# Optimization experiments

Hardware: AMD Instinct MI355X
Metric: run time of the kernel (lower is better)

## Reference

```python
import jax, jax.numpy as jnp
import numpy as np

B, A, T, NH, NEMB = 8, 32, 64, 256, 256
E = A * (A - 1)  # fully-connected directed edges, no self-loops


def _onehot_edges():
    # NRI-style: rows of off-diagonal pairs (send i -> recv j, i != j)
    send_idx, recv_idx = [], []
    for i in range(A):
        for j in range(A):
            if i != j:
                send_idx.append(i)
                recv_idx.append(j)
    rel_send = jax.nn.one_hot(jnp.array(send_idx), A, dtype=jnp.float32)
    rel_rec = jax.nn.one_hot(jnp.array(recv_idx), A, dtype=jnp.float32)
    return rel_rec, rel_send


def setup_inputs() -> dict:
    key = jax.random.key(0)
    k1, k2, k3 = jax.random.split(key, 3)
    h = jax.random.normal(k1, (B, A, T, NH), dtype=jnp.float32)
    rel_rec, rel_send = _onehot_edges()
    # nn.Linear(2*n_h, n_emb): W [n_emb, 2*n_h], b [n_emb]
    lim = 1.0 / np.sqrt(2 * NH)
    W = jax.random.uniform(k2, (NEMB, 2 * NH), minval=-lim, maxval=lim, dtype=jnp.float32)
    b = jax.random.uniform(k3, (NEMB,), minval=-lim, maxval=lim, dtype=jnp.float32)
    return {"h": h, "rel_rec": rel_rec, "rel_send": rel_send, "W": W, "b": b}


def reference(h, rel_rec, rel_send, W, b):
    # h: [B, A, T, NH]; rel_rec/rel_send: [E, A] one-hot selectors
    # Equivalent to reshape->batched matmul->reshape in the torch code,
    # expressed as a single contraction over atoms.
    receivers = jnp.einsum('ea,bath->beth', rel_rec, h)   # [B, E, T, NH]
    senders = jnp.einsum('ea,bath->beth', rel_send, h)    # [B, E, T, NH]
    edges = jnp.concatenate([senders, receivers], axis=-1)  # [B, E, T, 2*NH]
    return jnp.einsum('betf,of->beto', edges, W) + b        # [B, E, T, NEMB]
```

## Files before the change

kernel.cpp:

```cpp
#include <hip/hip_runtime.h>
#include <hip/hip_bf16.h>

using f32x4  = __attribute__((ext_vector_type(4))) float;
using bf16x8 = __attribute__((ext_vector_type(8))) short;
using s16x4  = __attribute__((ext_vector_type(4))) short;

constexpr int kB  = 8;
constexpr int kA  = 32;
constexpr int kT  = 64;
constexpr int kNH = 256;
constexpr int kNE = 256;
constexpr int kE  = kA * (kA - 1);
constexpr int kM  = kB * kA * kT;
constexpr int kK  = kNH;
constexpr int kN  = 2 * kNE;

__device__ __forceinline__ unsigned short rne_bf16(float f) {
    unsigned int u = __float_as_uint(f);
    u += 0x7fffu + ((u >> 16) & 1u);
    return (unsigned short)(u >> 16);
}
__device__ __forceinline__ float bf16_f32(unsigned short h) {
    return __uint_as_float(((unsigned int)h) << 16);
}
__device__ __forceinline__ void split3(float x, unsigned short& h, unsigned short& m,
                                       unsigned short& l) {
    h = rne_bf16(x);
    float r1 = x - bf16_f32(h);
    m = rne_bf16(r1);
    float r2 = r1 - bf16_f32(m);
    l = rne_bf16(r2);
}

__global__ __launch_bounds__(256) void k_split_h(const float* __restrict__ src,
                                                 unsigned short* __restrict__ d1,
                                                 unsigned short* __restrict__ d2,
                                                 unsigned short* __restrict__ d3) {
    int idx = blockIdx.x * 256 + threadIdx.x;
    f32x4 v = ((const f32x4*)src)[idx];
    s16x4 o1, o2, o3;
#pragma unroll
    for (int j = 0; j < 4; ++j) {
        unsigned short h, m, l;
        split3(v[j], h, m, l);
        o1[j] = (short)h; o2[j] = (short)m; o3[j] = (short)l;
    }
    *(s16x4*)(d1 + (size_t)idx * 4) = o1;
    *(s16x4*)(d2 + (size_t)idx * 4) = o2;
    *(s16x4*)(d3 + (size_t)idx * 4) = o3;
}

__global__ __launch_bounds__(256) void k_split_w(const float* __restrict__ W,
                                                 unsigned short* __restrict__ d1,
                                                 unsigned short* __restrict__ d2,
                                                 unsigned short* __restrict__ d3,
                                                 const float* __restrict__ rel_rec,
                                                 const float* __restrict__ rel_send,
                                                 int* __restrict__ ij2e) {
    int idx = blockIdx.x * 256 + threadIdx.x;
    int n  = idx >> 6;
    int k4 = (idx & 63) << 2;
    const float* s = (n < kNE) ? (W + (size_t)n * (2 * kNH) + k4)
                               : (W + (size_t)(n - kNE) * (2 * kNH) + kNH + k4);
    f32x4 v = *(const f32x4*)s;
    s16x4 o1, o2, o3;
#pragma unroll
    for (int j = 0; j < 4; ++j) {
        unsigned short h, m, l;
        split3(v[j], h, m, l);
        o1[j] = (short)h; o2[j] = (short)m; o3[j] = (short)l;
    }
    size_t off = (size_t)n * kK + k4;
    *(s16x4*)(d1 + off) = o1;
    *(s16x4*)(d2 + off) = o2;
    *(s16x4*)(d3 + off) = o3;

    if (blockIdx.x < 4) {
        int e = blockIdx.x * 256 + threadIdx.x;
        if (e < kE) {
            int ir = 0, is = 0;
            for (int a = 0; a < kA; ++a) {
                if (rel_rec[(size_t)e * kA + a]  > 0.5f) ir = a;
                if (rel_send[(size_t)e * kA + a] > 0.5f) is = a;
            }
            ij2e[is * kA + ir] = e;
        }
    }
}

#define GLL(g, l) __builtin_amdgcn_global_load_lds( \
    (const __attribute__((address_space(1))) void*)(g), \
    (__attribute__((address_space(3))) void*)(l), 16, 0, 0)

__global__ __launch_bounds__(256) void k_gemm3(const unsigned short* __restrict__ Ah,
                                               const unsigned short* __restrict__ Am,
                                               const unsigned short* __restrict__ Al,
                                               const unsigned short* __restrict__ Bh,
                                               const unsigned short* __restrict__ Bm,
                                               const unsigned short* __restrict__ Bl,
                                               float* __restrict__ P) {
    __shared__ unsigned short sAh[128 * 32], sAm[128 * 32], sAl[128 * 32];
    __shared__ unsigned short sBh[128 * 32], sBm[128 * 32], sBl[128 * 32];
    const int tid  = threadIdx.x;
    const int lane = tid & 63;
    const int wave = tid >> 6;
    const int wr = wave >> 1, wc = wave & 1;
    const int bid = blockIdx.x;
    const int bm  = (bid & 7) * 16 + ((bid >> 3) & 15);
    const int bn  = bid >> 7;

    const int sr   = tid >> 2;
    const int scb  = (tid & 3) << 4;
    const int scbs = scb ^ (((sr >> 1) & 3) << 4);
    const size_t rA  = (size_t)(bm * 128 + sr) * kK + (scbs >> 1);
    const size_t rB  = (size_t)(bn * 128 + sr) * kK + (scbs >> 1);
    const size_t rA1 = rA + (size_t)64 * kK;
    const size_t rB1 = rB + (size_t)64 * kK;
    const int l0 = tid * 8, l1 = 64 * 32 + tid * 8;

    const int fr  = lane & 15;
    const int fkb = (lane >> 4) << 4;
    const int swz = ((fr >> 1) & 3) << 4;

    f32x4 acc[4][4] = {};

    for (int kt = 0; kt < kK / 32; ++kt) {
        const int kk = kt * 32;
        __syncthreads();
        GLL(Ah + rA + kk, sAh + l0);  GLL(Ah + rA1 + kk, sAh + l1);
        GLL(Am + rA + kk, sAm + l0);  GLL(Am + rA1 + kk, sAm + l1);
        GLL(Al + rA + kk, sAl + l0);  GLL(Al + rA1 + kk, sAl + l1);
        GLL(Bh + rB + kk, sBh + l0);  GLL(Bh + rB1 + kk, sBh + l1);
        GLL(Bm + rB + kk, sBm + l0);  GLL(Bm + rB1 + kk, sBm + l1);
        GLL(Bl + rB + kk, sBl + l0);  GLL(Bl + rB1 + kk, sBl + l1);
        __syncthreads();

        bf16x8 ah[4], am[4], al[4], bh[4], bmf[4], bl[4];
#pragma unroll
        for (int mi = 0; mi < 4; ++mi) {
            int row = wr * 64 + mi * 16 + fr;
            int off = row * 64 + (fkb ^ swz);
            ah[mi] = *(const bf16x8*)((const char*)sAh + off);
            am[mi] = *(const bf16x8*)((const char*)sAm + off);
            al[mi] = *(const bf16x8*)((const char*)sAl + off);
        }
#pragma unroll
        for (int ni = 0; ni < 4; ++ni) {
            int row = wc * 64 + ni * 16 + fr;
            int off = row * 64 + (fkb ^ swz);
            bh[ni]  = *(const bf16x8*)((const char*)sBh + off);
            bmf[ni] = *(const bf16x8*)((const char*)sBm + off);
            bl[ni]  = *(const bf16x8*)((const char*)sBl + off);
        }
#pragma unroll
        for (int mi = 0; mi < 4; ++mi)
#pragma unroll
            for (int ni = 0; ni < 4; ++ni) {
                f32x4 c = acc[mi][ni];
                c = __builtin_amdgcn_mfma_f32_16x16x32_bf16(ah[mi], bh[ni],  c, 0, 0, 0);
                c = __builtin_amdgcn_mfma_f32_16x16x32_bf16(ah[mi], bmf[ni], c, 0, 0, 0);
                c = __builtin_amdgcn_mfma_f32_16x16x32_bf16(am[mi], bh[ni],  c, 0, 0, 0);
                c = __builtin_amdgcn_mfma_f32_16x16x32_bf16(ah[mi], bl[ni],  c, 0, 0, 0);
                c = __builtin_amdgcn_mfma_f32_16x16x32_bf16(al[mi], bh[ni],  c, 0, 0, 0);
                c = __builtin_amdgcn_mfma_f32_16x16x32_bf16(am[mi], bmf[ni], c, 0, 0, 0);
                acc[mi][ni] = c;
            }
    }

    const int col = lane & 15;
    const int rb  = (lane >> 4) << 2;
#pragma unroll
    for (int mi = 0; mi < 4; ++mi)
#pragma unroll
        for (int ni = 0; ni < 4; ++ni) {
            int n = bn * 128 + wc * 64 + ni * 16 + col;
#pragma unroll
            for (int r = 0; r < 4; ++r) {
                int m = bm * 128 + wr * 64 + mi * 16 + rb + r;
                P[(size_t)m * kN + n] = acc[mi][ni][r];
            }
        }
}

__global__ __launch_bounds__(256) void k_gather2(const float* __restrict__ P,
                                                 const float* __restrict__ bias,
                                                 const int* __restrict__ ij2e,
                                                 float* __restrict__ out) {
    const int bid = blockIdx.x;
    const int b  = bid & 7;
    const int gi = (bid >> 3) & 7;
    const int gj = bid >> 6;
    __shared__ int se[16];
    if (threadIdx.x < 16) {
        int si = threadIdx.x >> 2, rj = threadIdx.x & 3;
        int i = gi * 4 + si, j = gj * 4 + rj;
        se[threadIdx.x] = (i == j) ? -1 : ij2e[i * kA + j];
    }
    __syncthreads();
    int e[16];
#pragma unroll
    for (int k = 0; k < 16; ++k) e[k] = se[k];

    const int c  = threadIdx.x & 63;
    const int t0 = threadIdx.x >> 6;
    f32x4 bv = ((const f32x4*)bias)[c];
    const float* Pb = P + (size_t)(b * kA) * kT * kN;
    float* outb = out + (size_t)b * kE * kT * kNE;

    for (int t = t0; t < kT; t += 4) {
        f32x4 ps[4], pr[4];
#pragma unroll
        for (int si = 0; si < 4; ++si)
            ps[si] = *(const f32x4*)(Pb + ((size_t)(gi * 4 + si) * kT + t) * kN + c * 4);
#pragma unroll
        for (int rj = 0; rj < 4; ++rj)
            pr[rj] = *(const f32x4*)(Pb + ((size_t)(gj * 4 + rj) * kT + t) * kN + kNE + c * 4);
#pragma unroll
        for (int si = 0; si < 4; ++si)
#pragma unroll
            for (int rj = 0; rj < 4; ++rj) {
                int ee = e[si * 4 + rj];
                if (ee >= 0) {
                    f32x4 v = ps[si] + pr[rj] + bv;
                    __builtin_nontemporal_store(
                        v, (f32x4*)(outb + ((size_t)ee * kT + t) * kNE + c * 4));
                }
            }
    }
}

extern "C" void kernel_launch(void* const* d_in, const int* in_sizes, int n_in,
                              void* d_out, int out_size, void* d_ws, size_t ws_size,
                              hipStream_t stream) {
    const float* h    = (const float*)d_in[0];
    const float* rrec = (const float*)d_in[1];
    const float* rsnd = (const float*)d_in[2];
    const float* W    = (const float*)d_in[3];
    const float* bias = (const float*)d_in[4];
    float* out = (float*)d_out;

    char* ws = (char*)d_ws;
    const size_t MB = 1024 * 1024;
    unsigned short* Ah = (unsigned short*)(ws);
    unsigned short* Am = (unsigned short*)(ws + 8 * MB);
    unsigned short* Al = (unsigned short*)(ws + 16 * MB);
    unsigned short* Bh = (unsigned short*)(ws + 24 * MB);
    unsigned short* Bm = (unsigned short*)(ws + 24 * MB + 256 * 1024);
    unsigned short* Bl = (unsigned short*)(ws + 24 * MB + 512 * 1024);
    float* P   = (float*)(ws + 25 * MB);
    int* ij2e  = (int*)(ws + 57 * MB);

    k_split_h <<<dim3(kM * kK / (4 * 256)), dim3(256), 0, stream>>>(h, Ah, Am, Al);
    k_split_w <<<dim3(kN * kK / (4 * 256)), dim3(256), 0, stream>>>(W, Bh, Bm, Bl,
                                                                    rrec, rsnd, ij2e);
    k_gemm3   <<<dim3(512),                 dim3(256), 0, stream>>>(Ah, Am, Al, Bh, Bm, Bl, P);
    k_gather2 <<<dim3(512),                 dim3(256), 0, stream>>>(P, bias, ij2e, out);
}
```

Measured before the change: 140.7 us.

## Merge split kernels, remap GEMM blocks per XCD, double gather grid

The two bf16 split kernels become one launch, with block-index ranges choosing between h and W, which saves a kernel launch. The GEMM block-to-tile mapping is changed so each XCD handles 16 M-tiles across all 4 N-tiles, so the four N-tile blocks sharing an A tile run on the same XCD and can reuse it in L2. The gather kernel splits the T dimension in half and launches 1024 blocks instead of 512, giving more parallelism for the store-bound output write. The trade-off is fewer loop iterations per block and reading the edge table twice as often.

Result: no change. 139.7 us (-0.7%).

```diff
diff --git a/kernel.cpp b/kernel.cpp
--- a/kernel.cpp
+++ b/kernel.cpp
@@ -32,32 +32,35 @@
     l = rne_bf16(r2);
 }
 
-__global__ __launch_bounds__(256) void k_split_h(const float* __restrict__ src,
-                                                 unsigned short* __restrict__ d1,
-                                                 unsigned short* __restrict__ d2,
-                                                 unsigned short* __restrict__ d3) {
-    int idx = blockIdx.x * 256 + threadIdx.x;
-    f32x4 v = ((const f32x4*)src)[idx];
-    s16x4 o1, o2, o3;
-#pragma unroll
-    for (int j = 0; j < 4; ++j) {
-        unsigned short h, m, l;
-        split3(v[j], h, m, l);
-        o1[j] = (short)h; o2[j] = (short)m; o3[j] = (short)l;
-    }
-    *(s16x4*)(d1 + (size_t)idx * 4) = o1;
-    *(s16x4*)(d2 + (size_t)idx * 4) = o2;
-    *(s16x4*)(d3 + (size_t)idx * 4) = o3;
-}
-
-__global__ __launch_bounds__(256) void k_split_w(const float* __restrict__ W,
-                                                 unsigned short* __restrict__ d1,
-                                                 unsigned short* __restrict__ d2,
-                                                 unsigned short* __restrict__ d3,
-                                                 const float* __restrict__ rel_rec,
-                                                 const float* __restrict__ rel_send,
-                                                 int* __restrict__ ij2e) {
-    int idx = blockIdx.x * 256 + threadIdx.x;
+__global__ __launch_bounds__(256) void k_split_all(const float* __restrict__ hsrc,
+                                                   unsigned short* __restrict__ a1,
+                                                   unsigned short* __restrict__ a2,
+                                                   unsigned short* __restrict__ a3,
+                                                   const float* __restrict__ W,
+                                                   unsigned short* __restrict__ b1,
+                                                   unsigned short* __restrict__ b2,
+                                                   unsigned short* __restrict__ b3,
+                                                   const float* __restrict__ rel_rec,
+                                                   const float* __restrict__ rel_send,
+                                                   int* __restrict__ ij2e) {
+    const int bidx = blockIdx.x;
+    if (bidx < 4096) {
+        int idx = bidx * 256 + threadIdx.x;
+        f32x4 v = ((const f32x4*)hsrc)[idx];
+        s16x4 o1, o2, o3;
+#pragma unroll
+        for (int j = 0; j < 4; ++j) {
+            unsigned short h, m, l;
+            split3(v[j], h, m, l);
+            o1[j] = (short)h; o2[j] = (short)m; o3[j] = (short)l;
+        }
+        *(s16x4*)(a1 + (size_t)idx * 4) = o1;
+        *(s16x4*)(a2 + (size_t)idx * 4) = o2;
+        *(s16x4*)(a3 + (size_t)idx * 4) = o3;
+        return;
+    }
+    const int wb  = bidx - 4096;
+    int idx = wb * 256 + threadIdx.x;
     int n  = idx >> 6;
     int k4 = (idx & 63) << 2;
     const float* s = (n < kNE) ? (W + (size_t)n * (2 * kNH) + k4)
@@ -71,12 +74,12 @@
         o1[j] = (short)h; o2[j] = (short)m; o3[j] = (short)l;
     }
     size_t off = (size_t)n * kK + k4;
-    *(s16x4*)(d1 + off) = o1;
-    *(s16x4*)(d2 + off) = o2;
-    *(s16x4*)(d3 + off) = o3;
-
-    if (blockIdx.x < 4) {
-        int e = blockIdx.x * 256 + threadIdx.x;
+    *(s16x4*)(b1 + off) = o1;
+    *(s16x4*)(b2 + off) = o2;
+    *(s16x4*)(b3 + off) = o3;
+
+    if (wb < 4) {
+        int e = wb * 256 + threadIdx.x;
         if (e < kE) {
             int ir = 0, is = 0;
             for (int a = 0; a < kA; ++a) {
@@ -106,8 +109,10 @@
     const int wave = tid >> 6;
     const int wr = wave >> 1, wc = wave & 1;
     const int bid = blockIdx.x;
-    const int bm  = (bid & 7) * 16 + ((bid >> 3) & 15);
-    const int bn  = bid >> 7;
+    const int xcd = bid & 7;
+    const int idx = bid >> 3;
+    const int bn  = idx & 3;
+    const int bm  = xcd * 16 + (idx >> 2);
 
     const int sr   = tid >> 2;
     const int scb  = (tid & 3) << 4;
@@ -188,8 +193,9 @@
                                                  float* __restrict__ out) {
     const int bid = blockIdx.x;
     const int b  = bid & 7;
-    const int gi = (bid >> 3) & 7;
-    const int gj = bid >> 6;
+    const int th = (bid >> 3) & 1;
+    const int gi = (bid >> 4) & 7;
+    const int gj = bid >> 7;
     __shared__ int se[16];
     if (threadIdx.x < 16) {
         int si = threadIdx.x >> 2, rj = threadIdx.x & 3;
@@ -202,12 +208,12 @@
     for (int k = 0; k < 16; ++k) e[k] = se[k];
 
     const int c  = threadIdx.x & 63;
-    const int t0 = threadIdx.x >> 6;
+    const int t0 = th * 32 + (threadIdx.x >> 6);
     f32x4 bv = ((const f32x4*)bias)[c];
     const float* Pb = P + (size_t)(b * kA) * kT * kN;
     float* outb = out + (size_t)b * kE * kT * kNE;
 
-    for (int t = t0; t < kT; t += 4) {
+    for (int t = t0; t < th * 32 + 32; t += 4) {
         f32x4 ps[4], pr[4];
 #pragma unroll
         for (int si = 0; si < 4; ++si)
@@ -250,9 +256,9 @@
     float* P   = (float*)(ws + 25 * MB);
     int* ij2e  = (int*)(ws + 57 * MB);
 
-    k_split_h <<<dim3(kM * kK / (4 * 256)), dim3(256), 0, stream>>>(h, Ah, Am, Al);
-    k_split_w <<<dim3(kN * kK / (4 * 256)), dim3(256), 0, stream>>>(W, Bh, Bm, Bl,
-                                                                    rrec, rsnd, ij2e);
-    k_gemm3   <<<dim3(512),                 dim3(256), 0, stream>>>(Ah, Am, Al, Bh, Bm, Bl, P);
-    k_gather2 <<<dim3(512),                 dim3(256), 0, stream>>>(P, bias, ij2e, out);
-}
+    k_split_all<<<dim3(4096 + 128), dim3(256), 0, stream>>>(h, Ah, Am, Al,
+                                                            W, Bh, Bm, Bl,
+                                                            rrec, rsnd, ij2e);
+    k_gemm3    <<<dim3(512),        dim3(256), 0, stream>>>(Ah, Am, Al, Bh, Bm, Bl, P);
+    k_gather2  <<<dim3(1024),       dim3(256), 0, stream>>>(P, bias, ij2e, out);
+}
```
